# Optimization experiments

Hardware: AMD Instinct MI355X
Metric: run time of the kernel (lower is better)

## Reference

```python
import jax, jax.numpy as jnp
import numpy as np

WINDOW_SIZES = (128, 256, 512)
EMBED_DIM = 512
B, T = 128, 65536


def _branch_tokens(signal, W, b, w):
    # Conv1d(in=1, out=E, kernel=w, stride=w, padding=0) == non-overlapping
    # patch projection: (B, S, w) @ (w, E) with S = T // w.
    Bsz, Tlen = signal.shape
    S = Tlen // w
    patches = signal[:, : S * w].reshape(Bsz, S, w)
    return jnp.einsum('bsw,ew->bse', patches, W) + b  # (B, S, E)


def setup_inputs() -> dict:
    key = jax.random.key(0)
    ks = jax.random.split(key, 9)
    signal = jax.random.normal(ks[0], (B, T), dtype=jnp.float32)
    signal_mask = jax.random.randint(ks[1], (B, T), 0, 2).astype(bool)
    branch_idx = jax.random.randint(ks[2], (B,), 0, len(WINDOW_SIZES), dtype=jnp.int32)
    params = {}
    for i, w in enumerate(WINDOW_SIZES):
        params[f'W{i}'] = jax.random.normal(ks[3 + 2 * i], (EMBED_DIM, w), dtype=jnp.float32) * 0.02
        params[f'b{i}'] = jax.random.normal(ks[4 + 2 * i], (EMBED_DIM,), dtype=jnp.float32) * 0.02
    return {'signal': signal, 'signal_mask': signal_mask, 'branch_idx': branch_idx, **params}


def reference(signal, signal_mask, branch_idx, W0, b0, W1, b1, W2, b2):
    Bsz, Tlen = signal.shape
    Ws = (W0, W1, W2)
    bs = (b0, b1, b2)
    branch_S = [Tlen // w for w in WINDOW_SIZES]
    S_max = max(branch_S)
    # Compute every branch for every sample (faithful to the original module).
    padded = []
    for w, Wi, bi, Si in zip(WINDOW_SIZES, Ws, bs, branch_S):
        t = _branch_tokens(signal, Wi, bi, w)  # (B, Si, E)
        padded.append(jnp.pad(t, ((0, 0), (0, S_max - Si), (0, 0))))
    stacked = jnp.stack(padded)  # (n_branches, B, S_max, E)
    gathered = stacked[branch_idx, jnp.arange(Bsz)]  # (B, S_max, E)

    lengths = signal_mask.astype(jnp.int32).sum(axis=1)  # (B,)
    w_arr = jnp.asarray(WINDOW_SIZES, dtype=jnp.int32)
    S_arr = jnp.asarray(branch_S, dtype=jnp.int32)
    n_valid = jnp.minimum(lengths // w_arr[branch_idx],
                          jnp.minimum(S_arr[branch_idx], S_max))  # (B,)
    padding_mask = jnp.arange(S_max, dtype=jnp.int32)[None, :] < n_valid[:, None]  # (B, S_max)
    tokens = jnp.where(padding_mask[..., None], gathered, jnp.zeros((), signal.dtype))
    return tokens, padding_mask
```

## Files before the change

### kernel.cpp

```cpp
#include <hip/hip_runtime.h>
#include <hip/hip_bf16.h>

#define BATCH 128
#define TLEN  65536
#define EDIM  512
#define SMAX  512

typedef __attribute__((ext_vector_type(8))) short   bf16x8;
typedef __attribute__((ext_vector_type(4))) float   floatx4;
typedef __attribute__((ext_vector_type(8))) ushort  ushort8;

#define LDS_STRIDE 40

__device__ __forceinline__ ushort f2bf(float f) {
  __hip_bfloat16 h = __float2bfloat16(f);
  return *reinterpret_cast<ushort*>(&h);
}

__global__ __launch_bounds__(256) void mask_partial_kernel(
    const int* __restrict__ mask, int* __restrict__ part) {
  const int b = blockIdx.x, c = blockIdx.y, t = threadIdx.x;
  const int4* row = (const int4*)(mask + (size_t)b * TLEN + (size_t)c * 8192);
  int s = 0;
  #pragma unroll
  for (int i = 0; i < 8; ++i) {
    int4 v = row[t + i * 256];
    s += (v.x != 0) + (v.y != 0) + (v.z != 0) + (v.w != 0);
  }
  #pragma unroll
  for (int off = 32; off > 0; off >>= 1) s += __shfl_down(s, off);
  __shared__ int partial[4];
  if ((t & 63) == 0) partial[t >> 6] = s;
  __syncthreads();
  if (t == 0)
    part[b * 8 + c] = partial[0] + partial[1] + partial[2] + partial[3];
}

__global__ __launch_bounds__(256) void mask_final_kernel(
    const int* __restrict__ part, const int* __restrict__ branch_idx,
    int* __restrict__ n_valid, float* __restrict__ out_mask) {
  const int b = blockIdx.x, t = threadIdx.x;
  __shared__ int nv_sh;
  if (t == 0) {
    int len = 0;
    #pragma unroll
    for (int i = 0; i < 8; ++i) len += part[b * 8 + i];
    int w = 128 << branch_idx[b];
    int nv = len / w;
    n_valid[b] = nv;
    nv_sh = nv;
  }
  __syncthreads();
  const int nv = nv_sh;
  out_mask[(size_t)b * SMAX + t]       = (t < nv)       ? 1.0f : 0.0f;
  out_mask[(size_t)b * SMAX + 256 + t] = (256 + t < nv) ? 1.0f : 0.0f;
}

__global__ __launch_bounds__(256) void gemm_kernel(
    const float* __restrict__ signal, const int* __restrict__ branch_idx,
    const int* __restrict__ n_valid_arr,
    const float* __restrict__ W0, const float* __restrict__ bias0,
    const float* __restrict__ W1, const float* __restrict__ bias1,
    const float* __restrict__ W2, const float* __restrict__ bias2,
    float* __restrict__ out) {
  const int et = blockIdx.x;
  const int st = blockIdx.y;
  const int b  = blockIdx.z;
  const int t  = threadIdx.x;
  const int nv = n_valid_arr[b];
  const int s0 = st * 128;
  const int e0 = et * 128;
  float* outb = out + (size_t)b * SMAX * EDIM;

  if (s0 >= nv) {
    const float4 z = make_float4(0.f, 0.f, 0.f, 0.f);
    #pragma unroll
    for (int i = 0; i < 16; ++i) {
      int idx = t + i * 256;
      int r = idx >> 5, c = idx & 31;
      *(float4*)(outb + (size_t)(s0 + r) * EDIM + e0 + c * 4) = z;
    }
    return;
  }

  const int bi = branch_idx[b];
  const float* Wp = (bi == 0) ? W0 : (bi == 1) ? W1 : W2;
  const float* bp = (bi == 0) ? bias0 : (bi == 1) ? bias1 : bias2;
  const int w = 128 << bi;

  __shared__ __align__(16) ushort Abuf[128 * LDS_STRIDE];
  __shared__ __align__(16) ushort Bbuf[128 * LDS_STRIDE];

  const int wave   = t >> 6;
  const int lane   = t & 63;
  const int lane16 = lane & 15;
  const int quad   = lane >> 4;
  const int ws_ = (wave >> 1) * 64;
  const int we_ = (wave & 1) * 64;

  const int r = t >> 1, h = t & 1;
  const float* asrc = signal + (size_t)b * TLEN + (size_t)(s0 + r) * w + h * 16;
  const float* bsrc = Wp + (size_t)(e0 + r) * w + h * 16;
  ushort* adst = &Abuf[r * LDS_STRIDE + h * 16];
  ushort* bdst = &Bbuf[r * LDS_STRIDE + h * 16];

  floatx4 acc[4][4];
  #pragma unroll
  for (int i = 0; i < 4; ++i)
    #pragma unroll
    for (int j = 0; j < 4; ++j) acc[i][j] = (floatx4)(0.f);

  for (int k0 = 0; k0 < w; k0 += 32) {
    {
      const float4* a4 = (const float4*)(asrc + k0);
      const float4* b4 = (const float4*)(bsrc + k0);
      float4 av0 = a4[0], av1 = a4[1], av2 = a4[2], av3 = a4[3];
      float4 bv0 = b4[0], bv1 = b4[1], bv2 = b4[2], bv3 = b4[3];
      ushort8 p0, p1, q0, q1;
      p0[0]=f2bf(av0.x); p0[1]=f2bf(av0.y); p0[2]=f2bf(av0.z); p0[3]=f2bf(av0.w);
      p0[4]=f2bf(av1.x); p0[5]=f2bf(av1.y); p0[6]=f2bf(av1.z); p0[7]=f2bf(av1.w);
      p1[0]=f2bf(av2.x); p1[1]=f2bf(av2.y); p1[2]=f2bf(av2.z); p1[3]=f2bf(av2.w);
      p1[4]=f2bf(av3.x); p1[5]=f2bf(av3.y); p1[6]=f2bf(av3.z); p1[7]=f2bf(av3.w);
      q0[0]=f2bf(bv0.x); q0[1]=f2bf(bv0.y); q0[2]=f2bf(bv0.z); q0[3]=f2bf(bv0.w);
      q0[4]=f2bf(bv1.x); q0[5]=f2bf(bv1.y); q0[6]=f2bf(bv1.z); q0[7]=f2bf(bv1.w);
      q1[0]=f2bf(bv2.x); q1[1]=f2bf(bv2.y); q1[2]=f2bf(bv2.z); q1[3]=f2bf(bv2.w);
      q1[4]=f2bf(bv3.x); q1[5]=f2bf(bv3.y); q1[6]=f2bf(bv3.z); q1[7]=f2bf(bv3.w);
      *(ushort8*)adst = p0; *(ushort8*)(adst + 8) = p1;
      *(ushort8*)bdst = q0; *(ushort8*)(bdst + 8) = q1;
    }
    __syncthreads();
    bf16x8 af[4], bfr[4];
    #pragma unroll
    for (int i = 0; i < 4; ++i)
      af[i] = *(const bf16x8*)&Abuf[(ws_ + i * 16 + lane16) * LDS_STRIDE + quad * 8];
    #pragma unroll
    for (int j = 0; j < 4; ++j)
      bfr[j] = *(const bf16x8*)&Bbuf[(we_ + j * 16 + lane16) * LDS_STRIDE + quad * 8];
    #pragma unroll
    for (int i = 0; i < 4; ++i)
      #pragma unroll
      for (int j = 0; j < 4; ++j)
        acc[i][j] = __builtin_amdgcn_mfma_f32_16x16x32_bf16(af[i], bfr[j], acc[i][j], 0, 0, 0);
    __syncthreads();
  }

  float bval[4];
  #pragma unroll
  for (int j = 0; j < 4; ++j) bval[j] = bp[e0 + we_ + j * 16 + lane16];
  #pragma unroll
  for (int i = 0; i < 4; ++i) {
    #pragma unroll
    for (int rr = 0; rr < 4; ++rr) {
      const int s_row = s0 + ws_ + i * 16 + quad * 4 + rr;
      const bool valid = s_row < nv;
      float* op = outb + (size_t)s_row * EDIM + e0 + we_ + lane16;
      #pragma unroll
      for (int j = 0; j < 4; ++j)
        op[j * 16] = valid ? (acc[i][j][rr] + bval[j]) : 0.f;
    }
  }
}

extern "C" void kernel_launch(void* const* d_in, const int* in_sizes, int n_in,
                              void* d_out, int out_size, void* d_ws, size_t ws_size,
                              hipStream_t stream) {
  const float* signal = (const float*)d_in[0];
  const int*   mask   = (const int*)d_in[1];
  const int*   bidx   = (const int*)d_in[2];
  const float* W0 = (const float*)d_in[3];
  const float* b0 = (const float*)d_in[4];
  const float* W1 = (const float*)d_in[5];
  const float* b1 = (const float*)d_in[6];
  const float* W2 = (const float*)d_in[7];
  const float* b2 = (const float*)d_in[8];

  float* out_tokens = (float*)d_out;
  float* out_mask   = (float*)d_out + (size_t)BATCH * SMAX * EDIM;
  int*   n_valid    = (int*)d_ws;
  int*   part       = (int*)d_ws + 128;

  mask_partial_kernel<<<dim3(BATCH, 8), dim3(256), 0, stream>>>(mask, part);
  mask_final_kernel<<<dim3(BATCH), dim3(256), 0, stream>>>(part, bidx, n_valid, out_mask);
  gemm_kernel<<<dim3(4, 4, BATCH), dim3(256), 0, stream>>>(
      signal, bidx, n_valid, W0, b0, W1, b1, W2, b2, out_tokens);
}
```

Before: 259.2 us.

## Double-buffer LDS tiles with register prefetch and specialize GEMM per window size

```diff
diff --git a/kernel.cpp b/kernel.cpp
--- a/kernel.cpp
+++ b/kernel.cpp
@@ -11,10 +11,21 @@
 typedef __attribute__((ext_vector_type(8))) ushort  ushort8;
 
 #define LDS_STRIDE 40
+#define BUFSZ (128 * LDS_STRIDE)
 
 __device__ __forceinline__ ushort f2bf(float f) {
   __hip_bfloat16 h = __float2bfloat16(f);
   return *reinterpret_cast<ushort*>(&h);
+}
+
+__device__ __forceinline__ void cvt16(ushort* dst, float4 a, float4 b,
+                                      float4 c, float4 d) {
+  ushort8 p0, p1;
+  p0[0]=f2bf(a.x); p0[1]=f2bf(a.y); p0[2]=f2bf(a.z); p0[3]=f2bf(a.w);
+  p0[4]=f2bf(b.x); p0[5]=f2bf(b.y); p0[6]=f2bf(b.z); p0[7]=f2bf(b.w);
+  p1[0]=f2bf(c.x); p1[1]=f2bf(c.y); p1[2]=f2bf(c.z); p1[3]=f2bf(c.w);
+  p1[4]=f2bf(d.x); p1[5]=f2bf(d.y); p1[6]=f2bf(d.z); p1[7]=f2bf(d.w);
+  *(ushort8*)dst = p0; *(ushort8*)(dst + 8) = p1;
 }
 
 __global__ __launch_bounds__(256) void mask_partial_kernel(
@@ -54,6 +65,90 @@
   const int nv = nv_sh;
   out_mask[(size_t)b * SMAX + t]       = (t < nv)       ? 1.0f : 0.0f;
   out_mask[(size_t)b * SMAX + 256 + t] = (256 + t < nv) ? 1.0f : 0.0f;
+}
+
+template <int W>
+__device__ __forceinline__ void gemm_body(
+    const float* __restrict__ sigb, const float* __restrict__ Wp,
+    const float* __restrict__ bp, float* __restrict__ outb,
+    int nv, int s0, int e0, int t, ushort* Ab, ushort* Bb) {
+  constexpr int ITERS = W / 32;
+  const int wave   = t >> 6;
+  const int lane   = t & 63;
+  const int lane16 = lane & 15;
+  const int quad   = lane >> 4;
+  const int ws_ = (wave >> 1) * 64;
+  const int we_ = (wave & 1) * 64;
+  const int r = t >> 1, h = t & 1;
+
+  const float* asrc = sigb + (size_t)(s0 + r) * W + h * 16;
+  const float* bsrc = Wp + (size_t)(e0 + r) * W + h * 16;
+  ushort* adst = Ab + r * LDS_STRIDE + h * 16;
+  ushort* bdst = Bb + r * LDS_STRIDE + h * 16;
+
+  float4 av0, av1, av2, av3, bv0, bv1, bv2, bv3;
+  {
+    const float4* a4 = (const float4*)asrc;
+    const float4* b4 = (const float4*)bsrc;
+    av0 = a4[0]; av1 = a4[1]; av2 = a4[2]; av3 = a4[3];
+    bv0 = b4[0]; bv1 = b4[1]; bv2 = b4[2]; bv3 = b4[3];
+  }
+  cvt16(adst, av0, av1, av2, av3);
+  cvt16(bdst, bv0, bv1, bv2, bv3);
+  __syncthreads();
+
+  floatx4 acc[4][4];
+  #pragma unroll
+  for (int i = 0; i < 4; ++i)
+    #pragma unroll
+    for (int j = 0; j < 4; ++j) acc[i][j] = (floatx4)(0.f);
+
+  #pragma unroll
+  for (int k = 0; k < ITERS; ++k) {
+    const ushort* curA = Ab + (k & 1) * BUFSZ;
+    const ushort* curB = Bb + (k & 1) * BUFSZ;
+    if (k + 1 < ITERS) {
+      const float4* a4 = (const float4*)(asrc + (k + 1) * 32);
+      const float4* b4 = (const float4*)(bsrc + (k + 1) * 32);
+      av0 = a4[0]; av1 = a4[1]; av2 = a4[2]; av3 = a4[3];
+      bv0 = b4[0]; bv1 = b4[1]; bv2 = b4[2]; bv3 = b4[3];
+    }
+    bf16x8 af[4], bfr[4];
+    #pragma unroll
+    for (int i = 0; i < 4; ++i)
+      af[i] = *(const bf16x8*)&curA[(ws_ + i * 16 + lane16) * LDS_STRIDE + quad * 8];
+    #pragma unroll
+    for (int j = 0; j < 4; ++j)
+      bfr[j] = *(const bf16x8*)&curB[(we_ + j * 16 + lane16) * LDS_STRIDE + quad * 8];
+    #pragma unroll
+    for (int i = 0; i < 4; ++i)
+      #pragma unroll
+      for (int j = 0; j < 4; ++j)
+        acc[i][j] = __builtin_amdgcn_mfma_f32_16x16x32_bf16(af[i], bfr[j], acc[i][j], 0, 0, 0);
+    if (k + 1 < ITERS) {
+      ushort* nA = Ab + ((k + 1) & 1) * BUFSZ + r * LDS_STRIDE + h * 16;
+      ushort* nB = Bb + ((k + 1) & 1) * BUFSZ + r * LDS_STRIDE + h * 16;
+      cvt16(nA, av0, av1, av2, av3);
+      cvt16(nB, bv0, bv1, bv2, bv3);
+      __syncthreads();
+    }
+  }
+
+  float bval[4];
+  #pragma unroll
+  for (int j = 0; j < 4; ++j) bval[j] = bp[e0 + we_ + j * 16 + lane16];
+  #pragma unroll
+  for (int i = 0; i < 4; ++i) {
+    #pragma unroll
+    for (int rr = 0; rr < 4; ++rr) {
+      const int s_row = s0 + ws_ + i * 16 + quad * 4 + rr;
+      const bool valid = s_row < nv;
+      float* op = outb + (size_t)s_row * EDIM + e0 + we_ + lane16;
+      #pragma unroll
+      for (int j = 0; j < 4; ++j)
+        op[j * 16] = valid ? (acc[i][j][rr] + bval[j]) : 0.f;
+    }
+  }
 }
 
 __global__ __launch_bounds__(256) void gemm_kernel(
@@ -67,12 +162,13 @@
   const int st = blockIdx.y;
   const int b  = blockIdx.z;
   const int t  = threadIdx.x;
-  const int nv = n_valid_arr[b];
   const int s0 = st * 128;
   const int e0 = et * 128;
+  const int bi = branch_idx[b];
+  const int S_b = 512 >> bi;
   float* outb = out + (size_t)b * SMAX * EDIM;
 
-  if (s0 >= nv) {
+  if (s0 >= S_b) {
     const float4 z = make_float4(0.f, 0.f, 0.f, 0.f);
     #pragma unroll
     for (int i = 0; i < 16; ++i) {
@@ -83,81 +179,21 @@
     return;
   }
 
-  const int bi = branch_idx[b];
-  const float* Wp = (bi == 0) ? W0 : (bi == 1) ? W1 : W2;
-  const float* bp = (bi == 0) ? bias0 : (bi == 1) ? bias1 : bias2;
-  const int w = 128 << bi;
-
-  __shared__ __align__(16) ushort Abuf[128 * LDS_STRIDE];
-  __shared__ __align__(16) ushort Bbuf[128 * LDS_STRIDE];
-
-  const int wave   = t >> 6;
-  const int lane   = t & 63;
-  const int lane16 = lane & 15;
-  const int quad   = lane >> 4;
-  const int ws_ = (wave >> 1) * 64;
-  const int we_ = (wave & 1) * 64;
-
-  const int r = t >> 1, h = t & 1;
-  const float* asrc = signal + (size_t)b * TLEN + (size_t)(s0 + r) * w + h * 16;
-  const float* bsrc = Wp + (size_t)(e0 + r) * w + h * 16;
-  ushort* adst = &Abuf[r * LDS_STRIDE + h * 16];
-  ushort* bdst = &Bbuf[r * LDS_STRIDE + h * 16];
-
-  floatx4 acc[4][4];
-  #pragma unroll
-  for (int i = 0; i < 4; ++i)
-    #pragma unroll
-    for (int j = 0; j < 4; ++j) acc[i][j] = (floatx4)(0.f);
-
-  for (int k0 = 0; k0 < w; k0 += 32) {
-    {
-      const float4* a4 = (const float4*)(asrc + k0);
-      const float4* b4 = (const float4*)(bsrc + k0);
-      float4 av0 = a4[0], av1 = a4[1], av2 = a4[2], av3 = a4[3];
-      float4 bv0 = b4[0], bv1 = b4[1], bv2 = b4[2], bv3 = b4[3];
-      ushort8 p0, p1, q0, q1;
-      p0[0]=f2bf(av0.x); p0[1]=f2bf(av0.y); p0[2]=f2bf(av0.z); p0[3]=f2bf(av0.w);
-      p0[4]=f2bf(av1.x); p0[5]=f2bf(av1.y); p0[6]=f2bf(av1.z); p0[7]=f2bf(av1.w);
-      p1[0]=f2bf(av2.x); p1[1]=f2bf(av2.y); p1[2]=f2bf(av2.z); p1[3]=f2bf(av2.w);
-      p1[4]=f2bf(av3.x); p1[5]=f2bf(av3.y); p1[6]=f2bf(av3.z); p1[7]=f2bf(av3.w);
-      q0[0]=f2bf(bv0.x); q0[1]=f2bf(bv0.y); q0[2]=f2bf(bv0.z); q0[3]=f2bf(bv0.w);
-      q0[4]=f2bf(bv1.x); q0[5]=f2bf(bv1.y); q0[6]=f2bf(bv1.z); q0[7]=f2bf(bv1.w);
-      q1[0]=f2bf(bv2.x); q1[1]=f2bf(bv2.y); q1[2]=f2bf(bv2.z); q1[3]=f2bf(bv2.w);
-      q1[4]=f2bf(bv3.x); q1[5]=f2bf(bv3.y); q1[6]=f2bf(bv3.z); q1[7]=f2bf(bv3.w);
-      *(ushort8*)adst = p0; *(ushort8*)(adst + 8) = p1;
-      *(ushort8*)bdst = q0; *(ushort8*)(bdst + 8) = q1;
-    }
-    __syncthreads();
-    bf16x8 af[4], bfr[4];
-    #pragma unroll
-    for (int i = 0; i < 4; ++i)
-      af[i] = *(const bf16x8*)&Abuf[(ws_ + i * 16 + lane16) * LDS_STRIDE + quad * 8];
-    #pragma unroll
-    for (int j = 0; j < 4; ++j)
-      bfr[j] = *(const bf16x8*)&Bbuf[(we_ + j * 16 + lane16) * LDS_STRIDE + quad * 8];
-    #pragma unroll
-    for (int i = 0; i < 4; ++i)
-      #pragma unroll
-      for (int j = 0; j < 4; ++j)
-        acc[i][j] = __builtin_amdgcn_mfma_f32_16x16x32_bf16(af[i], bfr[j], acc[i][j], 0, 0, 0);
-    __syncthreads();
-  }
-
-  float bval[4];
-  #pragma unroll
-  for (int j = 0; j < 4; ++j) bval[j] = bp[e0 + we_ + j * 16 + lane16];
-  #pragma unroll
-  for (int i = 0; i < 4; ++i) {
-    #pragma unroll
-    for (int rr = 0; rr < 4; ++rr) {
-      const int s_row = s0 + ws_ + i * 16 + quad * 4 + rr;
-      const bool valid = s_row < nv;
-      float* op = outb + (size_t)s_row * EDIM + e0 + we_ + lane16;
-      #pragma unroll
-      for (int j = 0; j < 4; ++j)
-        op[j * 16] = valid ? (acc[i][j][rr] + bval[j]) : 0.f;
-    }
+  __shared__ __align__(16) ushort Ab[2 * BUFSZ];
+  __shared__ __align__(16) ushort Bb[2 * BUFSZ];
+  const int nv = n_valid_arr[b];
+  const float* sigb = signal + (size_t)b * TLEN;
+
+  switch (bi) {
+    case 0:
+      gemm_body<128>(sigb, W0, bias0, outb, nv, s0, e0, t, Ab, Bb);
+      break;
+    case 1:
+      gemm_body<256>(sigb, W1, bias1, outb, nv, s0, e0, t, Ab, Bb);
+      break;
+    default:
+      gemm_body<512>(sigb, W2, bias2, outb, nv, s0, e0, t, Ab, Bb);
+      break;
   }
 }
 
```

New measurement: 262.3 us. Within noise of the previous version (+1.2%).

## Load MFMA fragments directly from global memory and template GEMM on window size

Applied to the files above, without the earlier changes.

```diff
diff --git a/kernel.cpp b/kernel.cpp
--- a/kernel.cpp
+++ b/kernel.cpp
@@ -10,11 +10,16 @@
 typedef __attribute__((ext_vector_type(4))) float   floatx4;
 typedef __attribute__((ext_vector_type(8))) ushort  ushort8;
 
-#define LDS_STRIDE 40
-
 __device__ __forceinline__ ushort f2bf(float f) {
   __hip_bfloat16 h = __float2bfloat16(f);
   return *reinterpret_cast<ushort*>(&h);
+}
+
+__device__ __forceinline__ bf16x8 cvt_frag(float4 lo, float4 hi) {
+  ushort8 u;
+  u[0] = f2bf(lo.x); u[1] = f2bf(lo.y); u[2] = f2bf(lo.z); u[3] = f2bf(lo.w);
+  u[4] = f2bf(hi.x); u[5] = f2bf(hi.y); u[6] = f2bf(hi.z); u[7] = f2bf(hi.w);
+  return __builtin_bit_cast(bf16x8, u);
 }
 
 __global__ __launch_bounds__(256) void mask_partial_kernel(
@@ -56,53 +61,24 @@
   out_mask[(size_t)b * SMAX + 256 + t] = (256 + t < nv) ? 1.0f : 0.0f;
 }
 
-__global__ __launch_bounds__(256) void gemm_kernel(
-    const float* __restrict__ signal, const int* __restrict__ branch_idx,
-    const int* __restrict__ n_valid_arr,
-    const float* __restrict__ W0, const float* __restrict__ bias0,
-    const float* __restrict__ W1, const float* __restrict__ bias1,
-    const float* __restrict__ W2, const float* __restrict__ bias2,
-    float* __restrict__ out) {
-  const int et = blockIdx.x;
-  const int st = blockIdx.y;
-  const int b  = blockIdx.z;
-  const int t  = threadIdx.x;
-  const int nv = n_valid_arr[b];
-  const int s0 = st * 128;
-  const int e0 = et * 128;
-  float* outb = out + (size_t)b * SMAX * EDIM;
+template <int W>
+__device__ __forceinline__ void gemm_direct_body(
+    const float* __restrict__ sigb, const float* __restrict__ Wp,
+    const float* __restrict__ bp, float* __restrict__ outb,
+    int nv, int s0, int e0, int t) {
+  constexpr int ITERS = W / 32;
+  const int wave = t >> 6, lane = t & 63;
+  const int lane16 = lane & 15, quad = lane >> 4;
+  const int ws_ = (wave >> 1) * 64, we_ = (wave & 1) * 64;
 
-  if (s0 >= nv) {
-    const float4 z = make_float4(0.f, 0.f, 0.f, 0.f);
-    #pragma unroll
-    for (int i = 0; i < 16; ++i) {
-      int idx = t + i * 256;
-      int r = idx >> 5, c = idx & 31;
-      *(float4*)(outb + (size_t)(s0 + r) * EDIM + e0 + c * 4) = z;
-    }
-    return;
-  }
-
-  const int bi = branch_idx[b];
-  const float* Wp = (bi == 0) ? W0 : (bi == 1) ? W1 : W2;
-  const float* bp = (bi == 0) ? bias0 : (bi == 1) ? bias1 : bias2;
-  const int w = 128 << bi;
-
-  __shared__ __align__(16) ushort Abuf[128 * LDS_STRIDE];
-  __shared__ __align__(16) ushort Bbuf[128 * LDS_STRIDE];
-
-  const int wave   = t >> 6;
-  const int lane   = t & 63;
-  const int lane16 = lane & 15;
-  const int quad   = lane >> 4;
-  const int ws_ = (wave >> 1) * 64;
-  const int we_ = (wave & 1) * 64;
-
-  const int r = t >> 1, h = t & 1;
-  const float* asrc = signal + (size_t)b * TLEN + (size_t)(s0 + r) * w + h * 16;
-  const float* bsrc = Wp + (size_t)(e0 + r) * w + h * 16;
-  ushort* adst = &Abuf[r * LDS_STRIDE + h * 16];
-  ushort* bdst = &Bbuf[r * LDS_STRIDE + h * 16];
+  const float* ap[4];
+  const float* bpr[4];
+  #pragma unroll
+  for (int i = 0; i < 4; ++i)
+    ap[i] = sigb + (size_t)(s0 + ws_ + i * 16 + lane16) * W + quad * 8;
+  #pragma unroll
+  for (int j = 0; j < 4; ++j)
+    bpr[j] = Wp + (size_t)(e0 + we_ + j * 16 + lane16) * W + quad * 8;
 
   floatx4 acc[4][4];
   #pragma unroll
@@ -110,38 +86,29 @@
     #pragma unroll
     for (int j = 0; j < 4; ++j) acc[i][j] = (floatx4)(0.f);
 
-  for (int k0 = 0; k0 < w; k0 += 32) {
-    {
-      const float4* a4 = (const float4*)(asrc + k0);
-      const float4* b4 = (const float4*)(bsrc + k0);
-      float4 av0 = a4[0], av1 = a4[1], av2 = a4[2], av3 = a4[3];
-      float4 bv0 = b4[0], bv1 = b4[1], bv2 = b4[2], bv3 = b4[3];
-      ushort8 p0, p1, q0, q1;
-      p0[0]=f2bf(av0.x); p0[1]=f2bf(av0.y); p0[2]=f2bf(av0.z); p0[3]=f2bf(av0.w);
-      p0[4]=f2bf(av1.x); p0[5]=f2bf(av1.y); p0[6]=f2bf(av1.z); p0[7]=f2bf(av1.w);
-      p1[0]=f2bf(av2.x); p1[1]=f2bf(av2.y); p1[2]=f2bf(av2.z); p1[3]=f2bf(av2.w);
-      p1[4]=f2bf(av3.x); p1[5]=f2bf(av3.y); p1[6]=f2bf(av3.z); p1[7]=f2bf(av3.w);
-      q0[0]=f2bf(bv0.x); q0[1]=f2bf(bv0.y); q0[2]=f2bf(bv0.z); q0[3]=f2bf(bv0.w);
-      q0[4]=f2bf(bv1.x); q0[5]=f2bf(bv1.y); q0[6]=f2bf(bv1.z); q0[7]=f2bf(bv1.w);
-      q1[0]=f2bf(bv2.x); q1[1]=f2bf(bv2.y); q1[2]=f2bf(bv2.z); q1[3]=f2bf(bv2.w);
-      q1[4]=f2bf(bv3.x); q1[5]=f2bf(bv3.y); q1[6]=f2bf(bv3.z); q1[7]=f2bf(bv3.w);
-      *(ushort8*)adst = p0; *(ushort8*)(adst + 8) = p1;
-      *(ushort8*)bdst = q0; *(ushort8*)(bdst + 8) = q1;
+  #pragma unroll
+  for (int k = 0; k < ITERS; ++k) {
+    float4 al[4][2], bl[4][2];
+    #pragma unroll
+    for (int i = 0; i < 4; ++i) {
+      al[i][0] = *(const float4*)(ap[i] + k * 32);
+      al[i][1] = *(const float4*)(ap[i] + k * 32 + 4);
     }
-    __syncthreads();
+    #pragma unroll
+    for (int j = 0; j < 4; ++j) {
+      bl[j][0] = *(const float4*)(bpr[j] + k * 32);
+      bl[j][1] = *(const float4*)(bpr[j] + k * 32 + 4);
+    }
     bf16x8 af[4], bfr[4];
     #pragma unroll
-    for (int i = 0; i < 4; ++i)
-      af[i] = *(const bf16x8*)&Abuf[(ws_ + i * 16 + lane16) * LDS_STRIDE + quad * 8];
+    for (int i = 0; i < 4; ++i) af[i] = cvt_frag(al[i][0], al[i][1]);
     #pragma unroll
-    for (int j = 0; j < 4; ++j)
-      bfr[j] = *(const bf16x8*)&Bbuf[(we_ + j * 16 + lane16) * LDS_STRIDE + quad * 8];
+    for (int j = 0; j < 4; ++j) bfr[j] = cvt_frag(bl[j][0], bl[j][1]);
     #pragma unroll
     for (int i = 0; i < 4; ++i)
       #pragma unroll
       for (int j = 0; j < 4; ++j)
         acc[i][j] = __builtin_amdgcn_mfma_f32_16x16x32_bf16(af[i], bfr[j], acc[i][j], 0, 0, 0);
-    __syncthreads();
   }
 
   float bval[4];
@@ -158,6 +125,40 @@
       for (int j = 0; j < 4; ++j)
         op[j * 16] = valid ? (acc[i][j][rr] + bval[j]) : 0.f;
     }
+  }
+}
+
+__global__ __launch_bounds__(256) void gemm_kernel(
+    const float* __restrict__ signal, const int* __restrict__ branch_idx,
+    const int* __restrict__ n_valid_arr,
+    const float* __restrict__ W0, const float* __restrict__ bias0,
+    const float* __restrict__ W1, const float* __restrict__ bias1,
+    const float* __restrict__ W2, const float* __restrict__ bias2,
+    float* __restrict__ out) {
+  const int et = blockIdx.x, st = blockIdx.y, b = blockIdx.z;
+  const int t = threadIdx.x;
+  const int s0 = st * 128, e0 = et * 128;
+  const int bi = branch_idx[b];
+  const int S_b = 512 >> bi;
+  float* outb = out + (size_t)b * SMAX * EDIM;
+
+  if (s0 >= S_b) {
+    const float4 z = make_float4(0.f, 0.f, 0.f, 0.f);
+    #pragma unroll
+    for (int i = 0; i < 16; ++i) {
+      int idx = t + i * 256;
+      int r = idx >> 5, c = idx & 31;
+      *(float4*)(outb + (size_t)(s0 + r) * EDIM + e0 + c * 4) = z;
+    }
+    return;
+  }
+
+  const int nv = n_valid_arr[b];
+  const float* sigb = signal + (size_t)b * TLEN;
+  switch (bi) {
+    case 0:  gemm_direct_body<128>(sigb, W0, bias0, outb, nv, s0, e0, t); break;
+    case 1:  gemm_direct_body<256>(sigb, W1, bias1, outb, nv, s0, e0, t); break;
+    default: gemm_direct_body<512>(sigb, W2, bias2, outb, nv, s0, e0, t); break;
   }
 }
 
```

New measurement: 336.5 us. 29.8% more time.
